# Performance work log

Measured on AMD Instinct MI355X. Metric: run time of the kernel, lower is better.

The kernel has to match this reference:

```python
import jax, jax.numpy as jnp
import numpy as np

N_LEVELS = 128.0  # int8: [-128, 127]

def fake_quant(x):
    """Per-tensor int8 fixed-point fake quant (power-of-two scale), STE rounding."""
    maxabs = jnp.max(jnp.abs(x))
    # power-of-two scale covering maxabs, as in Brevitas *FixedPoint quantizers
    scale = jnp.exp2(jnp.ceil(jnp.log2(jnp.maximum(maxabs, 1e-10)))) / N_LEVELS
    scale = jax.lax.stop_gradient(scale)
    xs = x / scale
    q = jnp.clip(jnp.round(xs), -N_LEVELS, N_LEVELS - 1.0)
    q = xs + jax.lax.stop_gradient(q - xs)  # straight-through estimator
    return q * scale


def setup_inputs() -> dict:
    key = jax.random.key(0)
    k1, k2, k3, k4 = jax.random.split(key, 4)
    B, T, D, H = 512, 2048, 10, 20
    x = jax.random.normal(k1, (B, T, D), dtype=jnp.float32)
    h0 = jnp.zeros((B, H), dtype=jnp.float32)
    W_ih = jax.random.normal(k2, (H, D), dtype=jnp.float32) * 0.3
    W_hh = jax.random.normal(k3, (H, H), dtype=jnp.float32) * 0.2
    b = jax.random.normal(k4, (H,), dtype=jnp.float32) * 0.1
    return {"x": x, "h0": h0, "W_ih": W_ih, "W_hh": W_hh, "b": b}


def reference(x, h0, W_ih, W_hh, b):
    # io quant on input and initial state
    xq = fake_quant(x)
    h = fake_quant(h0)
    # weight / bias quant (per-tensor fixed point)
    Wi = fake_quant(W_ih)
    Wh = fake_quant(W_hh)
    bq = fake_quant(b)
    # precompute input-hidden contribution for all timesteps: [B,T,H]
    xW = jnp.einsum('btd,hd->bth', xq, Wi) + bq

    def step(h_prev, xw_t):
        acc = xw_t + h_prev @ Wh.T          # gate accumulation [B,H]
        acc = fake_quant(acc)               # gate_acc_quant
        h_new = jnp.tanh(acc)               # vanilla RNN nonlinearity
        out = fake_quant(h_new)             # io_quant on output/hidden
        return out, out

    xW_t = jnp.swapaxes(xW, 0, 1)           # [T,B,H]
    _, outs = jax.lax.scan(step, h, xW_t)   # outs: [T,B,H]
    return jnp.swapaxes(outs, 0, 1)         # batch_first output [B,T,H]
```

## Files before the change

### kernel.cpp

```cpp
#include <hip/hip_runtime.h>
#include <math.h>

#define BB 512
#define TT 2048
#define DD 10
#define HH 20
#define BH (BB*HH)

#define WS_AMAX     0
#define WS_PROD_XWI 4
#define WS_INV_SX   5
#define WS_S_H0     6
#define WS_INV_SH0  7
#define WS_S_WH     8
#define WS_BQ       16
#define WS_WIP      40
#define WS_WHP      104
#define WS_XW_OFF   4096

#define BAR() asm volatile("s_waitcnt lgkmcnt(0)\n\ts_barrier" ::: "memory")

__device__ __forceinline__ int dot4(int a, int b, int c) {
    return __builtin_amdgcn_sdot4(a, b, c, false);
}

__device__ __forceinline__ void p2s(float m, float* s, float* is) {
    m = fmaxf(m, 1e-10f);
    unsigned u = __float_as_uint(m);
    int k = (int)(u >> 23) - 127 + ((u & 0x7fffffu) ? 1 : 0);
    *s  = __uint_as_float((unsigned)(k + 120) << 23);
    *is = __uint_as_float((unsigned)(134 - k) << 23);
}

__device__ __forceinline__ float fmed3(float a, float b, float c) {
    return __builtin_amdgcn_fmed3f(a, b, c);
}

__device__ __forceinline__ int qlevel(float v, float inv) {
    return (int)fmed3(rintf(v * inv), -128.f, 127.f);
}

__device__ __forceinline__ int pack4(int a, int b, int c, int d) {
    return (a & 255) | ((b & 255) << 8) | ((c & 255) << 16) | ((d & 255) << 24);
}

__device__ __forceinline__ unsigned fenc(float x) {
    unsigned u = __float_as_uint(x);
    return u ^ (unsigned)(((int)u >> 31) | 0x80000000);
}
__device__ __forceinline__ float fdec(unsigned e) {
    unsigned mask = (~(unsigned)((int)e >> 31)) | 0x80000000u;
    return __uint_as_float(e ^ mask);
}

__device__ __forceinline__ unsigned umx(unsigned a, unsigned b) { return a > b ? a : b; }

__device__ __forceinline__ unsigned wave_umax(unsigned m) {
    unsigned t;
    t = (unsigned)__builtin_amdgcn_update_dpp(0, (int)m, 0x111, 0xf, 0xf, true); m = umx(m, t);
    t = (unsigned)__builtin_amdgcn_update_dpp(0, (int)m, 0x112, 0xf, 0xf, true); m = umx(m, t);
    t = (unsigned)__builtin_amdgcn_update_dpp(0, (int)m, 0x114, 0xf, 0xf, true); m = umx(m, t);
    t = (unsigned)__builtin_amdgcn_update_dpp(0, (int)m, 0x118, 0xf, 0xf, true); m = umx(m, t);
    t = (unsigned)__builtin_amdgcn_update_dpp(0, (int)m, 0x142, 0xa, 0xf, true); m = umx(m, t);
    t = (unsigned)__builtin_amdgcn_update_dpp(0, (int)m, 0x143, 0xc, 0xf, true); m = umx(m, t);
    return m;
}

__device__ __forceinline__ unsigned row_umax(unsigned m) {
    unsigned t;
    t = (unsigned)__builtin_amdgcn_update_dpp(0, (int)m, 0x121, 0xf, 0xf, true); m = umx(m, t);
    t = (unsigned)__builtin_amdgcn_update_dpp(0, (int)m, 0x122, 0xf, 0xf, true); m = umx(m, t);
    t = (unsigned)__builtin_amdgcn_update_dpp(0, (int)m, 0x124, 0xf, 0xf, true); m = umx(m, t);
    t = (unsigned)__builtin_amdgcn_update_dpp(0, (int)m, 0x128, 0xf, 0xf, true); m = umx(m, t);
    return m;
}

__device__ __forceinline__ void mk_hd(int PA, int PB, int PC, bool isLo, int* hd) {
    int QA = __builtin_amdgcn_update_dpp(0, PA, 0xB1, 0xf, 0xf, true);
    int QB = __builtin_amdgcn_update_dpp(0, PB, 0xB1, 0xf, 0xf, true);
    int QC = __builtin_amdgcn_update_dpp(0, PC, 0xB1, 0xf, 0xf, true);
    int XA = isLo ? PA : QA, XB = isLo ? PB : QB, XC = isLo ? PC : QC;
    int YA = isLo ? QA : PA, YB = isLo ? QB : PB, YC = isLo ? QC : PC;
    hd[0] = XA; hd[1] = XB;
    hd[2] = (XC & 0xFFFF) | (YA << 16);
    hd[3] = (int)((unsigned)YA >> 16) | (YB << 16);
    hd[4] = (int)((unsigned)YB >> 16) | (YC << 16);
}

__global__ void k_amax(const float* __restrict__ x, int n4, unsigned* amax) {
    int g = blockIdx.x * blockDim.x + threadIdx.x;
    int stride = gridDim.x * blockDim.x;
    const float4* xv = (const float4*)x;
    float m = 0.f;
    for (int i = g; i < n4; i += stride) {
        float4 v = xv[i];
        m = fmaxf(m, fmaxf(fmaxf(fabsf(v.x), fabsf(v.y)), fmaxf(fabsf(v.z), fabsf(v.w))));
    }
#pragma unroll
    for (int off = 32; off; off >>= 1) m = fmaxf(m, __shfl_xor(m, off, 64));
    if ((threadIdx.x & 63) == 0) atomicMax(amax, __float_as_uint(m));
}

__device__ float bmaxabs(const float* p, int n, float* red, int tid) {
    float m = 0.f;
    for (int i = tid; i < n; i += 256) m = fmaxf(m, fabsf(p[i]));
    red[tid] = m; __syncthreads();
    for (int s = 128; s; s >>= 1) {
        if (tid < s) red[tid] = fmaxf(red[tid], red[tid + s]);
        __syncthreads();
    }
    m = red[0]; __syncthreads();
    return m;
}

__global__ void k_prep(const float* __restrict__ Wi, const float* __restrict__ Wh,
                       const float* __restrict__ bias, const float* __restrict__ h0,
                       float* wsf, int* wsi) {
    __shared__ float red[256];
    __shared__ float hdr[4];
    int tid = threadIdx.x;
    float mwi = bmaxabs(Wi, HH * DD, red, tid);
    float mwh = bmaxabs(Wh, HH * HH, red, tid);
    float mb  = bmaxabs(bias, HH, red, tid);
    float mh0 = bmaxabs(h0, BH, red, tid);
    if (tid == 0) {
        float mx = __uint_as_float(((unsigned*)wsf)[WS_AMAX]);
        float sx, isx, swi, iswi, swh, iswh, sb, isb, sh0, ish0;
        p2s(mx,  &sx,  &isx);
        p2s(mwi, &swi, &iswi);
        p2s(mwh, &swh, &iswh);
        p2s(mb,  &sb,  &isb);
        p2s(mh0, &sh0, &ish0);
        wsf[WS_PROD_XWI] = sx * swi;
        wsf[WS_INV_SX]   = isx;
        wsf[WS_S_H0]     = sh0;
        wsf[WS_INV_SH0]  = ish0;
        wsf[WS_S_WH]     = swh;
        hdr[0] = iswi; hdr[1] = iswh; hdr[2] = sb; hdr[3] = isb;
    }
    __syncthreads();
    if (tid < HH) {
        float iswi = hdr[0], iswh = hdr[1], sb = hdr[2], isb = hdr[3];
        int lv[20];
#pragma unroll
        for (int d = 0; d < DD; ++d) lv[d] = qlevel(Wi[tid * DD + d], iswi);
        lv[10] = 0; lv[11] = 0;
#pragma unroll
        for (int k = 0; k < 3; ++k)
            wsi[WS_WIP + tid * 3 + k] = pack4(lv[4*k], lv[4*k+1], lv[4*k+2], lv[4*k+3]);
#pragma unroll
        for (int k = 0; k < HH; ++k) lv[k] = qlevel(Wh[tid * HH + k], iswh);
#pragma unroll
        for (int k = 0; k < 5; ++k)
            wsi[WS_WHP + tid * 5 + k] = pack4(lv[4*k], lv[4*k+1], lv[4*k+2], lv[4*k+3]);
        wsf[WS_BQ + tid] = (float)qlevel(bias[tid], isb) * sb;
    }
}

__global__ __launch_bounds__(256) void k_xw(const float* __restrict__ x,
                                            const float* __restrict__ wsf,
                                            const int* __restrict__ wsi,
                                            float* __restrict__ xw) {
    int g = blockIdx.x * 256 + threadIdx.x;
    int b = g & (BB - 1);
    int t = g >> 9;
    float isx  = wsf[WS_INV_SX];
    float prod = wsf[WS_PROD_XWI];
    const float2* xp = (const float2*)(x + ((size_t)b * TT + t) * DD);
    float xv[10];
#pragma unroll
    for (int k = 0; k < 5; ++k) { float2 v = xp[k]; xv[2*k] = v.x; xv[2*k+1] = v.y; }
    int lv[12];
#pragma unroll
    for (int d = 0; d < DD; ++d) lv[d] = qlevel(xv[d], isx);
    lv[10] = 0; lv[11] = 0;
    int xpk[3];
#pragma unroll
    for (int k = 0; k < 3; ++k) xpk[k] = pack4(lv[4*k], lv[4*k+1], lv[4*k+2], lv[4*k+3]);
    float res[20];
#pragma unroll
    for (int j = 0; j < HH; ++j) {
        int ai = 0;
#pragma unroll
        for (int k = 0; k < 3; ++k) ai = dot4(xpk[k], wsi[WS_WIP + j * 3 + k], ai);
        res[j] = (float)ai * prod + wsf[WS_BQ + j];
    }
    float4* op = (float4*)(xw + (size_t)t * BH + b * HH);
#pragma unroll
    for (int k = 0; k < 5; ++k)
        op[k] = make_float4(res[4*k], res[4*k+1], res[4*k+2], res[4*k+3]);
}

__global__ __launch_bounds__(1024, 4) void k_rnn(const float* __restrict__ h0,
                                                 const float* __restrict__ wsf,
                                                 const int* __restrict__ wsi,
                                                 float* __restrict__ xw) {
    __shared__ uint2 wred[16];
    __shared__ float bc[4];
    __shared__ int2 lut[256];
    const int tid = threadIdx.x;
    const int b = tid >> 1;
    const int jb = (tid & 1) * 10;
    const bool isLo = (tid & 1) == 0;
    const float s_wh = wsf[WS_S_WH];
    float sprod = wsf[WS_S_H0] * s_wh;

    int whp[50];
#pragma unroll
    for (int jj = 0; jj < 10; ++jj)
#pragma unroll
        for (int k = 0; k < 5; ++k)
            whp[jj * 5 + k] = wsi[WS_WHP + (jb + jj) * 5 + k];

    int hd[5];
    {
        float ish0 = wsf[WS_INV_SH0];
        const float2* hp = (const float2*)(h0 + b * HH + jb);
        int lv[10];
#pragma unroll
        for (int k = 0; k < 5; ++k) {
            float2 v = hp[k];
            lv[2*k]   = qlevel(v.x, ish0);
            lv[2*k+1] = qlevel(v.y, ish0);
        }
        mk_hd(pack4(lv[0], lv[1], lv[2], lv[3]),
              pack4(lv[4], lv[5], lv[6], lv[7]),
              (lv[8] & 255) | ((lv[9] & 255) << 8), isLo, hd);
    }
    float xwA[10];
    {
        const float2* p = (const float2*)(xw + b * HH + jb);
#pragma unroll
        for (int k = 0; k < 5; ++k) { float2 v = p[k]; xwA[2*k] = v.x; xwA[2*k+1] = v.y; }
    }
    const float2* pf = (const float2*)(xw + (size_t)BH + b * HH + jb);
    float2*       po = (float2*)(xw + b * HH + jb);

    for (int t = 0; t < TT; ++t) {
        float xwB[10];
        if (t + 1 < TT) {
#pragma unroll
            for (int k = 0; k < 5; ++k) { float2 v = pf[k]; xwB[2*k] = v.x; xwB[2*k+1] = v.y; }
        }
        float acc[10];
#pragma unroll
        for (int jj = 0; jj < 10; ++jj) {
            int ai = 0;
#pragma unroll
            for (int k = 0; k < 5; ++k) ai = dot4(hd[k], whp[jj * 5 + k], ai);
            acc[jj] = fmaf((float)ai, sprod, xwA[jj]);
        }
        float mx = acc[0], mn = acc[0];
#pragma unroll
        for (int jj = 1; jj < 10; ++jj) { mx = fmaxf(mx, acc[jj]); mn = fminf(mn, acc[jj]); }
        unsigned ea = wave_umax(fenc(mx));
        unsigned eb = wave_umax(fenc(-mn));
        if ((tid & 63) == 63) wred[tid >> 6] = make_uint2(ea, eb);
        BAR();
        float isa, sh;
        if (tid < 256) {
            uint2 wp = wred[tid & 15];
            float ma = fdec(row_umax(wp.x));
            float nm = fdec(row_umax(wp.y));
            float sa; p2s(fmaxf(ma, nm), &sa, &isa);
            float lp = fmed3(rintf(ma * isa), -128.f, 127.f);
            float ln = fmed3(rintf(-nm * isa), -128.f, 127.f);
            float mlvl = fmaxf(fabsf(lp), fabsf(ln));
            float mh = tanhf(mlvl * sa);
            float ish; p2s(mh, &sh, &ish);
            sprod = sh * s_wh;
            float tq = tanhf((float)(tid - 128) * sa);
            int lv = (int)fmed3(rintf(tq * ish), -128.f, 127.f);
            lut[tid] = make_int2(lv, __float_as_int((float)lv * sh));
            if (tid == 0) { bc[0] = isa; bc[1] = sh; bc[2] = sprod; }
        }
        BAR();
        if (tid >= 256) { isa = bc[0]; sh = bc[1]; sprod = bc[2]; }
        int ql[10];
#pragma unroll
        for (int k = 0; k < 5; ++k) {
            int qa = (int)fmed3(rintf(acc[2*k]   * isa), -128.f, 127.f);
            int qb = (int)fmed3(rintf(acc[2*k+1] * isa), -128.f, 127.f);
            int2 ea2 = lut[qa + 128];
            int2 eb2 = lut[qb + 128];
            ql[2*k]   = ea2.x;
            ql[2*k+1] = eb2.x;
            po[k] = make_float2(__int_as_float(ea2.y), __int_as_float(eb2.y));
        }
        mk_hd(pack4(ql[0], ql[1], ql[2], ql[3]),
              pack4(ql[4], ql[5], ql[6], ql[7]),
              (ql[8] & 255) | ((ql[9] & 255) << 8), isLo, hd);
#pragma unroll
        for (int jj = 0; jj < 10; ++jj) xwA[jj] = xwB[jj];
        pf += BH / 2;
        po += BH / 2;
    }
}

__global__ __launch_bounds__(256) void k_tr(const float* __restrict__ src, float* __restrict__ out) {
    __shared__ float tile[16 * 16 * HH];
    int t0 = blockIdx.x * 16, b0 = blockIdx.y * 16;
    for (int i = threadIdx.x; i < 16 * 16 * HH; i += 256) {
        int r = i / (16 * HH), c = i % (16 * HH);
        tile[i] = src[(size_t)(t0 + r) * BH + b0 * HH + c];
    }
    __syncthreads();
    for (int i = threadIdx.x; i < 16 * 16 * HH; i += 256) {
        int bb = i / (16 * HH), rj = i % (16 * HH);
        int r = rj / HH, j = rj % HH;
        out[(size_t)(b0 + bb) * (TT * HH) + (t0 + r) * HH + j] = tile[r * (16 * HH) + bb * HH + j];
    }
}

extern "C" void kernel_launch(void* const* d_in, const int* in_sizes, int n_in,
                              void* d_out, int out_size, void* d_ws, size_t ws_size,
                              hipStream_t stream) {
    const float* x    = (const float*)d_in[0];
    const float* h0   = (const float*)d_in[1];
    const float* Wi   = (const float*)d_in[2];
    const float* Wh   = (const float*)d_in[3];
    const float* bias = (const float*)d_in[4];
    float* out = (float*)d_out;

    char* w = (char*)d_ws;
    float* wsf = (float*)w;
    int* wsi = (int*)w;
    unsigned* amax = (unsigned*)w;
    float* xw = (float*)(w + WS_XW_OFF);

    hipMemsetAsync(d_ws, 0, 64, stream);
    int n = in_sizes[0];
    k_amax<<<2048, 256, 0, stream>>>(x, n / 4, amax);
    k_prep<<<1, 256, 0, stream>>>(Wi, Wh, bias, h0, wsf, wsi);
    k_xw<<<(BB * TT) / 256, 256, 0, stream>>>(x, wsf, wsi, xw);
    k_rnn<<<1, 1024, 0, stream>>>(h0, wsf, wsi, xw);
    k_tr<<<dim3(TT / 16, BB / 16), 256, 0, stream>>>(xw, out);
}
```

Measured before the change: 4.576 ms.

## Map one batch row per thread in the RNN kernel, dropping lane-pair exchanges

The recurrent kernel now runs 512 threads, one per batch row with all 20 hidden units, where it used to run 1024 threads with two threads per row. This removes the DPP swaps that rebuilt the packed hidden state across lane pairs and the shared-memory broadcast of scales, since every thread now computes the scale chain itself from an 8-wave reduction. The loop is unrolled by two with ping-pong prefetch buffers. In exchange each thread holds 100 weight registers and twice the dot products, which lengthens the serial per-step critical path and raises register pressure.

```diff
diff --git a/kernel.cpp b/kernel.cpp
--- a/kernel.cpp
+++ b/kernel.cpp
@@ -66,25 +66,12 @@
     return m;
 }
 
-__device__ __forceinline__ unsigned row_umax(unsigned m) {
+__device__ __forceinline__ unsigned oct_umax(unsigned m) {
     unsigned t;
     t = (unsigned)__builtin_amdgcn_update_dpp(0, (int)m, 0x121, 0xf, 0xf, true); m = umx(m, t);
     t = (unsigned)__builtin_amdgcn_update_dpp(0, (int)m, 0x122, 0xf, 0xf, true); m = umx(m, t);
     t = (unsigned)__builtin_amdgcn_update_dpp(0, (int)m, 0x124, 0xf, 0xf, true); m = umx(m, t);
-    t = (unsigned)__builtin_amdgcn_update_dpp(0, (int)m, 0x128, 0xf, 0xf, true); m = umx(m, t);
     return m;
-}
-
-__device__ __forceinline__ void mk_hd(int PA, int PB, int PC, bool isLo, int* hd) {
-    int QA = __builtin_amdgcn_update_dpp(0, PA, 0xB1, 0xf, 0xf, true);
-    int QB = __builtin_amdgcn_update_dpp(0, PB, 0xB1, 0xf, 0xf, true);
-    int QC = __builtin_amdgcn_update_dpp(0, PC, 0xB1, 0xf, 0xf, true);
-    int XA = isLo ? PA : QA, XB = isLo ? PB : QB, XC = isLo ? PC : QC;
-    int YA = isLo ? QA : PA, YB = isLo ? QB : PB, YC = isLo ? QC : PC;
-    hd[0] = XA; hd[1] = XB;
-    hd[2] = (XC & 0xFFFF) | (YA << 16);
-    hd[3] = (int)((unsigned)YA >> 16) | (YB << 16);
-    hd[4] = (int)((unsigned)YB >> 16) | (YC << 16);
 }
 
 __global__ void k_amax(const float* __restrict__ x, int n4, unsigned* amax) {
@@ -191,109 +178,112 @@
         op[k] = make_float4(res[4*k], res[4*k+1], res[4*k+2], res[4*k+3]);
 }
 
-__global__ __launch_bounds__(1024, 4) void k_rnn(const float* __restrict__ h0,
-                                                 const float* __restrict__ wsf,
-                                                 const int* __restrict__ wsi,
-                                                 float* __restrict__ xw) {
-    __shared__ uint2 wred[16];
-    __shared__ float bc[4];
+__global__ __launch_bounds__(512, 2) void k_rnn(const float* __restrict__ h0,
+                                                const float* __restrict__ wsf,
+                                                const int* __restrict__ wsi,
+                                                float* __restrict__ xw) {
+    __shared__ uint2 wred[8];
     __shared__ int2 lut[256];
     const int tid = threadIdx.x;
-    const int b = tid >> 1;
-    const int jb = (tid & 1) * 10;
-    const bool isLo = (tid & 1) == 0;
+    const int b = tid;
     const float s_wh = wsf[WS_S_WH];
     float sprod = wsf[WS_S_H0] * s_wh;
 
-    int whp[50];
-#pragma unroll
-    for (int jj = 0; jj < 10; ++jj)
-#pragma unroll
-        for (int k = 0; k < 5; ++k)
-            whp[jj * 5 + k] = wsi[WS_WHP + (jb + jj) * 5 + k];
+    int whp[100];
+#pragma unroll
+    for (int i = 0; i < 100; ++i) whp[i] = wsi[WS_WHP + i];
 
     int hd[5];
     {
         float ish0 = wsf[WS_INV_SH0];
-        const float2* hp = (const float2*)(h0 + b * HH + jb);
-        int lv[10];
+        const float4* hp = (const float4*)(h0 + b * HH);
+        int lv[20];
 #pragma unroll
         for (int k = 0; k < 5; ++k) {
-            float2 v = hp[k];
-            lv[2*k]   = qlevel(v.x, ish0);
-            lv[2*k+1] = qlevel(v.y, ish0);
-        }
-        mk_hd(pack4(lv[0], lv[1], lv[2], lv[3]),
-              pack4(lv[4], lv[5], lv[6], lv[7]),
-              (lv[8] & 255) | ((lv[9] & 255) << 8), isLo, hd);
-    }
-    float xwA[10];
+            float4 v = hp[k];
+            lv[4*k]   = qlevel(v.x, ish0);
+            lv[4*k+1] = qlevel(v.y, ish0);
+            lv[4*k+2] = qlevel(v.z, ish0);
+            lv[4*k+3] = qlevel(v.w, ish0);
+        }
+#pragma unroll
+        for (int k = 0; k < 5; ++k)
+            hd[k] = pack4(lv[4*k], lv[4*k+1], lv[4*k+2], lv[4*k+3]);
+    }
+
+    float xw0[20], xw1[20];
     {
-        const float2* p = (const float2*)(xw + b * HH + jb);
-#pragma unroll
-        for (int k = 0; k < 5; ++k) { float2 v = p[k]; xwA[2*k] = v.x; xwA[2*k+1] = v.y; }
-    }
-    const float2* pf = (const float2*)(xw + (size_t)BH + b * HH + jb);
-    float2*       po = (float2*)(xw + b * HH + jb);
-
-    for (int t = 0; t < TT; ++t) {
-        float xwB[10];
+        const float4* p = (const float4*)(xw + b * HH);
+#pragma unroll
+        for (int k = 0; k < 5; ++k) {
+            float4 v = p[k];
+            xw0[4*k] = v.x; xw0[4*k+1] = v.y; xw0[4*k+2] = v.z; xw0[4*k+3] = v.w;
+        }
+    }
+    const float4* pf = (const float4*)(xw + (size_t)BH + b * HH);
+    float4*       po = (float4*)(xw + b * HH);
+
+    auto step = [&](int t, float (&xa)[20], float (&xb)[20]) {
         if (t + 1 < TT) {
 #pragma unroll
-            for (int k = 0; k < 5; ++k) { float2 v = pf[k]; xwB[2*k] = v.x; xwB[2*k+1] = v.y; }
-        }
-        float acc[10];
-#pragma unroll
-        for (int jj = 0; jj < 10; ++jj) {
+            for (int k = 0; k < 5; ++k) {
+                float4 v = pf[k];
+                xb[4*k] = v.x; xb[4*k+1] = v.y; xb[4*k+2] = v.z; xb[4*k+3] = v.w;
+            }
+        }
+        float acc[20];
+#pragma unroll
+        for (int j = 0; j < HH; ++j) {
             int ai = 0;
 #pragma unroll
-            for (int k = 0; k < 5; ++k) ai = dot4(hd[k], whp[jj * 5 + k], ai);
-            acc[jj] = fmaf((float)ai, sprod, xwA[jj]);
+            for (int k = 0; k < 5; ++k) ai = dot4(hd[k], whp[j * 5 + k], ai);
+            acc[j] = fmaf((float)ai, sprod, xa[j]);
         }
         float mx = acc[0], mn = acc[0];
 #pragma unroll
-        for (int jj = 1; jj < 10; ++jj) { mx = fmaxf(mx, acc[jj]); mn = fminf(mn, acc[jj]); }
+        for (int j = 1; j < HH; ++j) { mx = fmaxf(mx, acc[j]); mn = fminf(mn, acc[j]); }
         unsigned ea = wave_umax(fenc(mx));
         unsigned eb = wave_umax(fenc(-mn));
         if ((tid & 63) == 63) wred[tid >> 6] = make_uint2(ea, eb);
         BAR();
-        float isa, sh;
+        uint2 wp = wred[tid & 7];
+        float ma = fdec(oct_umax(wp.x));
+        float nm = fdec(oct_umax(wp.y));
+        float sa, isa; p2s(fmaxf(ma, nm), &sa, &isa);
+        float lp = fmed3(rintf(ma * isa), -128.f, 127.f);
+        float ln = fmed3(rintf(-nm * isa), -128.f, 127.f);
+        float mlvl = fmaxf(fabsf(lp), fabsf(ln));
+        float mh = tanhf(mlvl * sa);
+        float sh, ish; p2s(mh, &sh, &ish);
+        sprod = sh * s_wh;
         if (tid < 256) {
-            uint2 wp = wred[tid & 15];
-            float ma = fdec(row_umax(wp.x));
-            float nm = fdec(row_umax(wp.y));
-            float sa; p2s(fmaxf(ma, nm), &sa, &isa);
-            float lp = fmed3(rintf(ma * isa), -128.f, 127.f);
-            float ln = fmed3(rintf(-nm * isa), -128.f, 127.f);
-            float mlvl = fmaxf(fabsf(lp), fabsf(ln));
-            float mh = tanhf(mlvl * sa);
-            float ish; p2s(mh, &sh, &ish);
-            sprod = sh * s_wh;
             float tq = tanhf((float)(tid - 128) * sa);
             int lv = (int)fmed3(rintf(tq * ish), -128.f, 127.f);
             lut[tid] = make_int2(lv, __float_as_int((float)lv * sh));
-            if (tid == 0) { bc[0] = isa; bc[1] = sh; bc[2] = sprod; }
         }
         BAR();
-        if (tid >= 256) { isa = bc[0]; sh = bc[1]; sprod = bc[2]; }
-        int ql[10];
-#pragma unroll
-        for (int k = 0; k < 5; ++k) {
-            int qa = (int)fmed3(rintf(acc[2*k]   * isa), -128.f, 127.f);
-            int qb = (int)fmed3(rintf(acc[2*k+1] * isa), -128.f, 127.f);
-            int2 ea2 = lut[qa + 128];
-            int2 eb2 = lut[qb + 128];
-            ql[2*k]   = ea2.x;
-            ql[2*k+1] = eb2.x;
-            po[k] = make_float2(__int_as_float(ea2.y), __int_as_float(eb2.y));
-        }
-        mk_hd(pack4(ql[0], ql[1], ql[2], ql[3]),
-              pack4(ql[4], ql[5], ql[6], ql[7]),
-              (ql[8] & 255) | ((ql[9] & 255) << 8), isLo, hd);
-#pragma unroll
-        for (int jj = 0; jj < 10; ++jj) xwA[jj] = xwB[jj];
-        pf += BH / 2;
-        po += BH / 2;
+        int ql[20];
+        float ov[20];
+#pragma unroll
+        for (int j = 0; j < HH; ++j) {
+            int qi = (int)fmed3(rintf(acc[j] * isa), -128.f, 127.f);
+            int2 e = lut[qi + 128];
+            ql[j] = e.x;
+            ov[j] = __int_as_float(e.y);
+        }
+#pragma unroll
+        for (int k = 0; k < 5; ++k)
+            po[k] = make_float4(ov[4*k], ov[4*k+1], ov[4*k+2], ov[4*k+3]);
+#pragma unroll
+        for (int k = 0; k < 5; ++k)
+            hd[k] = pack4(ql[4*k], ql[4*k+1], ql[4*k+2], ql[4*k+3]);
+        pf += BH / 4;
+        po += BH / 4;
+    };
+
+    for (int t = 0; t < TT; t += 2) {
+        step(t, xw0, xw1);
+        step(t + 1, xw1, xw0);
     }
 }
 
@@ -333,6 +323,6 @@
     k_amax<<<2048, 256, 0, stream>>>(x, n / 4, amax);
     k_prep<<<1, 256, 0, stream>>>(Wi, Wh, bias, h0, wsf, wsi);
     k_xw<<<(BB * TT) / 256, 256, 0, stream>>>(x, wsf, wsi, xw);
-    k_rnn<<<1, 1024, 0, stream>>>(h0, wsf, wsi, xw);
+    k_rnn<<<1, 512, 0, stream>>>(h0, wsf, wsi, xw);
     k_tr<<<dim3(TT / 16, BB / 16), 256, 0, stream>>>(xw, out);
 }
```

Result: slower. 5.721 ms (+25.0%).

## Split hidden halves across block halves and exchange state via LDS

Applied to the files above, without the earlier changes.

Remaps threads so each half of the block computes one half of the hidden units for all batch rows. Weight rows become wave-uniform, so they can load as scalars. The neighbor-lane DPP exchange of quantized hidden state is replaced by an LDS write, an extra barrier and a read from the partner thread. The time loop is manually unrolled by two with ping-pong xw buffers to avoid register copies. The change trades the DPP shuffle for an extra block-wide barrier per step, which could cost more in this latency-bound recurrence.

```diff
diff --git a/kernel.cpp b/kernel.cpp
--- a/kernel.cpp
+++ b/kernel.cpp
@@ -73,18 +73,6 @@
     t = (unsigned)__builtin_amdgcn_update_dpp(0, (int)m, 0x124, 0xf, 0xf, true); m = umx(m, t);
     t = (unsigned)__builtin_amdgcn_update_dpp(0, (int)m, 0x128, 0xf, 0xf, true); m = umx(m, t);
     return m;
-}
-
-__device__ __forceinline__ void mk_hd(int PA, int PB, int PC, bool isLo, int* hd) {
-    int QA = __builtin_amdgcn_update_dpp(0, PA, 0xB1, 0xf, 0xf, true);
-    int QB = __builtin_amdgcn_update_dpp(0, PB, 0xB1, 0xf, 0xf, true);
-    int QC = __builtin_amdgcn_update_dpp(0, PC, 0xB1, 0xf, 0xf, true);
-    int XA = isLo ? PA : QA, XB = isLo ? PB : QB, XC = isLo ? PC : QC;
-    int YA = isLo ? QA : PA, YB = isLo ? QB : PB, YC = isLo ? QC : PC;
-    hd[0] = XA; hd[1] = XB;
-    hd[2] = (XC & 0xFFFF) | (YA << 16);
-    hd[3] = (int)((unsigned)YA >> 16) | (YB << 16);
-    hd[4] = (int)((unsigned)YB >> 16) | (YC << 16);
 }
 
 __global__ void k_amax(const float* __restrict__ x, int n4, unsigned* amax) {
@@ -191,56 +179,60 @@
         op[k] = make_float4(res[4*k], res[4*k+1], res[4*k+2], res[4*k+3]);
 }
 
-__global__ __launch_bounds__(1024, 4) void k_rnn(const float* __restrict__ h0,
-                                                 const float* __restrict__ wsf,
-                                                 const int* __restrict__ wsi,
-                                                 float* __restrict__ xw) {
+__global__ __launch_bounds__(1024)
+__attribute__((amdgpu_waves_per_eu(4, 4)))
+void k_rnn(const float* __restrict__ h0,
+           const float* __restrict__ wsf,
+           const int* __restrict__ wsi,
+           float* __restrict__ xw) {
     __shared__ uint2 wred[16];
     __shared__ float bc[4];
     __shared__ int2 lut[256];
+    __shared__ int4 hx[1024];
     const int tid = threadIdx.x;
-    const int b = tid >> 1;
-    const int jb = (tid & 1) * 10;
-    const bool isLo = (tid & 1) == 0;
+    const int b = tid & 511;
+    const int hf = tid >> 9;
+    const int jb = hf * 10;
+    const int jbu = __builtin_amdgcn_readfirstlane(jb);
     const float s_wh = wsf[WS_S_WH];
     float sprod = wsf[WS_S_H0] * s_wh;
 
     int whp[50];
-#pragma unroll
-    for (int jj = 0; jj < 10; ++jj)
-#pragma unroll
-        for (int k = 0; k < 5; ++k)
-            whp[jj * 5 + k] = wsi[WS_WHP + (jb + jj) * 5 + k];
+    const int* wrow = wsi + WS_WHP + jbu * 5;
+#pragma unroll
+    for (int i = 0; i < 50; ++i) whp[i] = wrow[i];
 
     int hd[5];
     {
         float ish0 = wsf[WS_INV_SH0];
-        const float2* hp = (const float2*)(h0 + b * HH + jb);
-        int lv[10];
+        const float4* hp = (const float4*)(h0 + b * HH);
+        int lv[20];
 #pragma unroll
         for (int k = 0; k < 5; ++k) {
-            float2 v = hp[k];
-            lv[2*k]   = qlevel(v.x, ish0);
-            lv[2*k+1] = qlevel(v.y, ish0);
-        }
-        mk_hd(pack4(lv[0], lv[1], lv[2], lv[3]),
-              pack4(lv[4], lv[5], lv[6], lv[7]),
-              (lv[8] & 255) | ((lv[9] & 255) << 8), isLo, hd);
-    }
-    float xwA[10];
+            float4 v = hp[k];
+            lv[4*k]   = qlevel(v.x, ish0);
+            lv[4*k+1] = qlevel(v.y, ish0);
+            lv[4*k+2] = qlevel(v.z, ish0);
+            lv[4*k+3] = qlevel(v.w, ish0);
+        }
+#pragma unroll
+        for (int k = 0; k < 5; ++k)
+            hd[k] = pack4(lv[4*k], lv[4*k+1], lv[4*k+2], lv[4*k+3]);
+    }
+
+    float xw0[10], xw1[10];
     {
         const float2* p = (const float2*)(xw + b * HH + jb);
 #pragma unroll
-        for (int k = 0; k < 5; ++k) { float2 v = p[k]; xwA[2*k] = v.x; xwA[2*k+1] = v.y; }
+        for (int k = 0; k < 5; ++k) { float2 v = p[k]; xw0[2*k] = v.x; xw0[2*k+1] = v.y; }
     }
     const float2* pf = (const float2*)(xw + (size_t)BH + b * HH + jb);
     float2*       po = (float2*)(xw + b * HH + jb);
 
-    for (int t = 0; t < TT; ++t) {
-        float xwB[10];
+    auto step = [&](int t, float (&xa)[10], float (&xb)[10]) {
         if (t + 1 < TT) {
 #pragma unroll
-            for (int k = 0; k < 5; ++k) { float2 v = pf[k]; xwB[2*k] = v.x; xwB[2*k+1] = v.y; }
+            for (int k = 0; k < 5; ++k) { float2 v = pf[k]; xb[2*k] = v.x; xb[2*k+1] = v.y; }
         }
         float acc[10];
 #pragma unroll
@@ -248,7 +240,7 @@
             int ai = 0;
 #pragma unroll
             for (int k = 0; k < 5; ++k) ai = dot4(hd[k], whp[jj * 5 + k], ai);
-            acc[jj] = fmaf((float)ai, sprod, xwA[jj]);
+            acc[jj] = fmaf((float)ai, sprod, xa[jj]);
         }
         float mx = acc[0], mn = acc[0];
 #pragma unroll
@@ -275,25 +267,39 @@
             if (tid == 0) { bc[0] = isa; bc[1] = sh; bc[2] = sprod; }
         }
         BAR();
-        if (tid >= 256) { isa = bc[0]; sh = bc[1]; sprod = bc[2]; }
+        if (tid >= 256) { isa = bc[0]; sprod = bc[2]; }
         int ql[10];
 #pragma unroll
         for (int k = 0; k < 5; ++k) {
             int qa = (int)fmed3(rintf(acc[2*k]   * isa), -128.f, 127.f);
             int qb = (int)fmed3(rintf(acc[2*k+1] * isa), -128.f, 127.f);
-            int2 ea2 = lut[qa + 128];
-            int2 eb2 = lut[qb + 128];
-            ql[2*k]   = ea2.x;
-            ql[2*k+1] = eb2.x;
-            po[k] = make_float2(__int_as_float(ea2.y), __int_as_float(eb2.y));
-        }
-        mk_hd(pack4(ql[0], ql[1], ql[2], ql[3]),
-              pack4(ql[4], ql[5], ql[6], ql[7]),
-              (ql[8] & 255) | ((ql[9] & 255) << 8), isLo, hd);
-#pragma unroll
-        for (int jj = 0; jj < 10; ++jj) xwA[jj] = xwB[jj];
+            int2 e0 = lut[qa + 128];
+            int2 e1 = lut[qb + 128];
+            ql[2*k]   = e0.x;
+            ql[2*k+1] = e1.x;
+            po[k] = make_float2(__int_as_float(e0.y), __int_as_float(e1.y));
+        }
+        {
+            int P0 = pack4(ql[0], ql[1], ql[2], ql[3]);
+            int P1 = pack4(ql[4], ql[5], ql[6], ql[7]);
+            int P2 = (ql[8] & 255) | ((ql[9] & 255) << 8);
+            hx[tid] = make_int4(P0, P1, P2, 0);
+            BAR();
+            int4 q = hx[tid ^ 512];
+            int X0 = hf ? q.x : P0, X1 = hf ? q.y : P1, X2 = hf ? q.z : P2;
+            int Y0 = hf ? P0 : q.x, Y1 = hf ? P1 : q.y, Y2 = hf ? P2 : q.z;
+            hd[0] = X0; hd[1] = X1;
+            hd[2] = (X2 & 0xFFFF) | (Y0 << 16);
+            hd[3] = (int)((unsigned)Y0 >> 16) | (Y1 << 16);
+            hd[4] = (int)((unsigned)Y1 >> 16) | (Y2 << 16);
+        }
         pf += BH / 2;
         po += BH / 2;
+    };
+
+    for (int t = 0; t < TT; t += 2) {
+        step(t, xw0, xw1);
+        step(t + 1, xw1, xw0);
     }
 }
 
```

New measurement: 5.929 ms. 1.3x slower.
